# Optimization experiments

Measured on AMD Instinct MI355X. Metric: run time of the kernel, lower is better.

Reference implementation:

```python
import jax, jax.numpy as jnp
import numpy as np

LN_EPS = 1e-5
MASK_FILL = -1e9


def setup_inputs() -> dict:
    key = jax.random.key(0)
    ks = jax.random.split(key, 10)
    B, L, D, H, O, K = 128, 2048, 128, 256, 128, 64
    return {
        "sequence_emb": jax.random.normal(ks[0], (B, L, D), jnp.float32),
        "mask": jax.random.randint(ks[1], (B, L), 0, 2, jnp.int32),
        "target_emb": jax.random.normal(ks[2], (B, D), jnp.float32),
        "pos_table": jax.random.normal(ks[3], (10000, D), jnp.float32) * 0.02,
        "W_imp1": jax.random.normal(ks[4], (3 * D, H), jnp.float32) * (1.0 / np.sqrt(3 * D)),
        "b_imp1": jnp.zeros((H,), jnp.float32),
        "W_imp2": jax.random.normal(ks[5], (H, 1), jnp.float32) * (1.0 / np.sqrt(H)),
        "b_imp2": jnp.zeros((1,), jnp.float32),
        "W_enc1": jax.random.normal(ks[6], (2 * D, H), jnp.float32) * (1.0 / np.sqrt(2 * D)),
        "b_enc1": jnp.zeros((H,), jnp.float32),
        "W_enc2": jax.random.normal(ks[7], (H, O), jnp.float32) * (1.0 / np.sqrt(H)),
        "b_enc2": jnp.zeros((O,), jnp.float32),
        "ln_gamma": jnp.ones((O,), jnp.float32),
        "ln_beta": jnp.zeros((O,), jnp.float32),
        "top_k": K,
    }


def reference(sequence_emb, mask, target_emb, pos_table, W_imp1, b_imp1, W_imp2,
              b_imp2, W_enc1, b_enc1, W_enc2, b_enc2, ln_gamma, ln_beta, top_k):
    B, L, D = sequence_emb.shape
    # position embedding lookup (positions identical across batch -> keep (L,D) and broadcast)
    positions = jnp.minimum(jnp.arange(L), pos_table.shape[0] - 1)
    pos_emb = jnp.broadcast_to(pos_table[positions][None], (B, L, D))
    combined = jnp.concatenate([sequence_emb, pos_emb], axis=-1)          # (B,L,2D)
    tgt = jnp.broadcast_to(target_emb[:, None, :], (B, L, D))
    imp_in = jnp.concatenate([combined, tgt], axis=-1)                    # (B,L,3D)
    # importance MLP -> scalar score per event
    h = jax.nn.relu(imp_in @ W_imp1 + b_imp1)
    scores = (h @ W_imp2 + b_imp2)[..., 0]                                # (B,L)
    scores = jnp.where(mask == 0, MASK_FILL, scores)
    # masked top-k, then gather in chronological (sorted-index) order
    topk_values, topk_indices = jax.lax.top_k(scores, top_k)              # (B,K)
    idx_sorted = jnp.sort(topk_indices, axis=-1)
    sel = jnp.take_along_axis(combined, idx_sorted[..., None], axis=1)    # (B,K,2D)
    encoded = jax.nn.relu(sel @ W_enc1 + b_enc1) @ W_enc2 + b_enc2        # (B,K,O)
    # reorder scores to match sorted index order (torch: gather by argsort of indices)
    order = jnp.argsort(topk_indices, axis=-1)
    topk_scores = jnp.take_along_axis(topk_values, order, axis=-1)
    attn = jax.nn.softmax(topk_scores, axis=-1)                           # (B,K)
    pooled = jnp.einsum('bk,bkd->bd', attn, encoded)                      # (B,O)
    mu = jnp.mean(pooled, axis=-1, keepdims=True)
    var = jnp.var(pooled, axis=-1, keepdims=True)
    return (pooled - mu) * jax.lax.rsqrt(var + LN_EPS) * ln_gamma + ln_beta
```

## Files before the change

kernel.cpp:

```cpp
#include <hip/hip_runtime.h>
#include <hip/hip_bf16.h>

namespace {
constexpr int NB = 128;
constexpr int NL = 2048;
constexpr int ND = 128;
constexpr int NH = 256;
constexpr int NO = 128;
constexpr int NK = 64;
constexpr int MCAP = 192;
constexpr int HTHR = 96;
constexpr int BLOOP = 8;
constexpr float MASK_FILL_F = -1e9f;
constexpr float LN_EPS_F = 1e-5f;
}

typedef __attribute__((ext_vector_type(8))) short bf16x8;
typedef __attribute__((ext_vector_type(4))) float f32x4;

__device__ __forceinline__ unsigned short bf16rne(float x) {
  unsigned u = __float_as_uint(x);
  return (unsigned short)((u + 0x7FFFu + ((u >> 16) & 1u)) >> 16);
}

__global__ __launch_bounds__(256) void k_prep(
    const float* __restrict__ W1, const float* __restrict__ pos,
    const float* __restrict__ tgt, const float* __restrict__ b1,
    const float* __restrict__ We1, const float* __restrict__ We2,
    unsigned short* __restrict__ W1aT, float* __restrict__ P,
    float* __restrict__ T, unsigned short* __restrict__ We1T,
    unsigned short* __restrict__ We2T) {
  const int blk = blockIdx.x, t = threadIdx.x;
  if (blk < ND) {
    W1aT[(size_t)t * ND + blk] = bf16rne(W1[(size_t)blk * NH + t]);
    return;
  }
  if (blk >= ND + NL + NB) {
    const int b2 = blk - (ND + NL + NB);
    if (b2 < 256) {
      We1T[(size_t)t * 256 + b2] = bf16rne(We1[(size_t)b2 * NH + t]);
    } else {
      const int d = b2 - 256;
      if (t < NO) We2T[(size_t)t * 256 + d] = bf16rne(We2[(size_t)d * NO + t]);
    }
    return;
  }
  int r, w_off, add_bias;
  const float* src;
  float* out;
  if (blk < ND + NL) {
    r = blk - ND; src = pos; out = P; w_off = ND; add_bias = 1;
  } else {
    r = blk - (ND + NL); src = tgt; out = T; w_off = 2 * ND; add_bias = 0;
  }
  __shared__ float row[ND];
  if (t < ND) row[t] = src[(size_t)r * ND + t];
  __syncthreads();
  float acc = add_bias ? b1[t] : 0.0f;
#pragma unroll 8
  for (int d = 0; d < ND; ++d)
    acc = fmaf(row[d], W1[(size_t)(w_off + d) * NH + t], acc);
  out[(size_t)r * NH + t] = acc;
}

__global__ __launch_bounds__(512, 2) void k_scores_mfma(
    const float* __restrict__ seq, const int* __restrict__ mask,
    const unsigned short* __restrict__ W1aT, const float* __restrict__ w2,
    const float* __restrict__ b2, const float* __restrict__ b1,
    const float* __restrict__ T, float* __restrict__ scores) {
  const int l0 = blockIdx.x * 128;
  const int b0 = blockIdx.y * BLOOP;
  const int t = threadIdx.x;
  const int lane = t & 63;
  const int w = t >> 6;
  const int wh = w & 3;
  const int wl = w >> 2;
  const int lh = lane & 15;
  const int kq = lane >> 4;

  __shared__ unsigned short sSeq[2][128 * 128];
  __shared__ float sRed[4][128];

  bf16x8 a[4][4];
#pragma unroll
  for (int ks = 0; ks < 4; ++ks)
#pragma unroll
    for (int mt = 0; mt < 4; ++mt)
      a[ks][mt] = *(const bf16x8*)(
          W1aT + (size_t)(wh * 64 + mt * 16 + lh) * ND + ks * 32 + kq * 8);

  float4 wv[4], b1v[4];
#pragma unroll
  for (int mt = 0; mt < 4; ++mt) {
    wv[mt] = *(const float4*)(w2 + wh * 64 + mt * 16 + kq * 4);
    b1v[mt] = *(const float4*)(b1 + wh * 64 + mt * 16 + kq * 4);
  }
  const float b2v = b2[0];

  ushort4 pf[8];
  auto prefetch = [&](int bb) {
    const float4* g = (const float4*)(seq + ((size_t)bb * NL + l0) * ND);
#pragma unroll
    for (int i = 0; i < 8; ++i) {
      const float4 f = g[t + i * 512];
      pf[i].x = bf16rne(f.x); pf[i].y = bf16rne(f.y);
      pf[i].z = bf16rne(f.z); pf[i].w = bf16rne(f.w);
    }
  };
  auto commit = [&](unsigned short* dst) {
#pragma unroll
    for (int i = 0; i < 8; ++i) {
      const int v = t + i * 512;
      const int row = v >> 5;
      const int c8 = (v & 31) * 8;
      const int off = (row << 8) + (c8 ^ ((row & 15) << 4));
      *(ushort4*)((char*)dst + off) = pf[i];
    }
  };

  prefetch(b0);
  commit((unsigned short*)sSeq[0]);
  __syncthreads();

#pragma unroll 1
  for (int j = 0; j < BLOOP; ++j) {
    const int b = b0 + j;
    unsigned short* cSeq = (unsigned short*)sSeq[j & 1];
    unsigned short* nSeq = (unsigned short*)sSeq[(j & 1) ^ 1];

    if (j + 1 < BLOOP) prefetch(b + 1);

    float4 Tv[4];
#pragma unroll
    for (int mt = 0; mt < 4; ++mt)
      Tv[mt] = *(const float4*)(T + (size_t)b * NH + wh * 64 + mt * 16 + kq * 4);

    f32x4 acc[4][4];
#pragma unroll
    for (int mt = 0; mt < 4; ++mt)
#pragma unroll
      for (int nt = 0; nt < 4; ++nt) acc[mt][nt] = (f32x4){0.f, 0.f, 0.f, 0.f};

#pragma unroll
    for (int ks = 0; ks < 4; ++ks) {
      bf16x8 Bf[4];
#pragma unroll
      for (int nt = 0; nt < 4; ++nt) {
        const int row = wl * 64 + nt * 16 + lh;
        const int off = (row << 8) + (((ks << 6) + (kq << 4)) ^ ((row & 15) << 4));
        Bf[nt] = *(const bf16x8*)((const char*)cSeq + off);
      }
#pragma unroll
      for (int mt = 0; mt < 4; ++mt)
#pragma unroll
        for (int nt = 0; nt < 4; ++nt)
          acc[mt][nt] = __builtin_amdgcn_mfma_f32_16x16x32_bf16(
              a[ks][mt], Bf[nt], acc[mt][nt], 0, 0, 0);
    }
    __syncthreads();
    if (j + 1 < BLOOP) commit(nSeq);

    float p[4] = {0.f, 0.f, 0.f, 0.f};
#pragma unroll
    for (int mt = 0; mt < 4; ++mt) {
#pragma unroll
      for (int nt = 0; nt < 4; ++nt) {
        float z;
        z = acc[mt][nt][0] + Tv[mt].x + b1v[mt].x; p[nt] = fmaf(fmaxf(z, 0.f), wv[mt].x, p[nt]);
        z = acc[mt][nt][1] + Tv[mt].y + b1v[mt].y; p[nt] = fmaf(fmaxf(z, 0.f), wv[mt].y, p[nt]);
        z = acc[mt][nt][2] + Tv[mt].z + b1v[mt].z; p[nt] = fmaf(fmaxf(z, 0.f), wv[mt].z, p[nt]);
        z = acc[mt][nt][3] + Tv[mt].w + b1v[mt].w; p[nt] = fmaf(fmaxf(z, 0.f), wv[mt].w, p[nt]);
      }
    }
#pragma unroll
    for (int nt = 0; nt < 4; ++nt) {
      float v = p[nt];
      v += __shfl_xor(v, 16);
      v += __shfl_xor(v, 32);
      if (lane < 16) sRed[wh][wl * 64 + nt * 16 + lane] = v;
    }
    __syncthreads();
    if (t < 128) {
      const int l = l0 + t;
      float sc = sRed[0][t] + sRed[1][t] + sRed[2][t] + sRed[3][t] + b2v;
      if (mask[(size_t)b * NL + l] == 0) sc = MASK_FILL_F;
      scores[(size_t)b * NL + l] = sc;
    }
  }
}

__global__ __launch_bounds__(1024, 4) void k_select3(
    const float* __restrict__ scores, const float* __restrict__ seq,
    const int* __restrict__ mask, const float* __restrict__ W1,
    const float* __restrict__ w2, const float* __restrict__ b2,
    const float* __restrict__ P, const float* __restrict__ T,
    int* __restrict__ idx_sorted, float* __restrict__ attn) {
  const int b = blockIdx.x, t = threadIdx.x;
  __shared__ float s_stage[128 * ND];
  unsigned* hist = (unsigned*)s_stage;
  __shared__ unsigned chunk[256];
  __shared__ int sB;
  __shared__ unsigned sCntHi, sCntB, sN;
  __shared__ int s_cand[MCAP];
  __shared__ float s_cs[MCAP];
  __shared__ unsigned long long s_key[MCAP];
  __shared__ int sel_l[NK];
  __shared__ float sel_v[NK];
  __shared__ int srt_l[NK];
  __shared__ float srt_v[NK];

  for (int i = t; i < 4096; i += 1024) hist[i] = 0;
  if (t == 0) { sCntHi = 0; sCntB = 0; }
  __syncthreads();
  unsigned key2[2];
#pragma unroll
  for (int i = 0; i < 2; ++i) {
    unsigned u = __float_as_uint(scores[(size_t)b * NL + t + i * 1024]);
    u = (u & 0x80000000u) ? ~u : (u | 0x80000000u);
    key2[i] = u;
    atomicAdd(&hist[u >> 20], 1u);
  }
  __syncthreads();
  if (t < 256) {
    unsigned s = 0;
#pragma unroll 4
    for (int j = 0; j < 16; ++j) s += hist[t * 16 + j];
    chunk[t] = s;
  }
  __syncthreads();
  if (t == 0) {
    unsigned cum = 0;
    int c = 255;
    for (; c > 0; --c) {
      if (cum + chunk[c] >= (unsigned)HTHR) break;
      cum += chunk[c];
    }
    int bin = c * 16 + 15;
    for (; bin > c * 16; --bin) {
      if (cum + hist[bin] >= (unsigned)HTHR) break;
      cum += hist[bin];
    }
    sB = bin;
  }
  __syncthreads();
  const unsigned B = (unsigned)sB;
#pragma unroll
  for (int i = 0; i < 2; ++i) {
    if ((key2[i] >> 20) > B) {
      unsigned pos = atomicAdd(&sCntHi, 1u);
      s_cand[pos] = t + i * 1024;
    }
  }
  __syncthreads();
  const unsigned hi = sCntHi;
#pragma unroll
  for (int i = 0; i < 2; ++i) {
    if ((key2[i] >> 20) == B) {
      unsigned pos = atomicAdd(&sCntB, 1u);
      if (hi + pos < (unsigned)MCAP) s_cand[hi + pos] = t + i * 1024;
    }
  }
  __syncthreads();
  if (t == 0) {
    unsigned n = sCntHi + sCntB;
    sN = (n < (unsigned)MCAP) ? n : (unsigned)MCAP;
  }
  __syncthreads();
  const int n = (int)sN;

  const int hg = t & 63;
  const int rg = t >> 6;
  const float4* Wp = (const float4*)W1;
  const float4 wvq = ((const float4*)w2)[hg];
  const float4 Tvq = ((const float4*)(T + (size_t)b * NH))[hg];
  const float b2v = b2[0];
#pragma unroll 1
  for (int pass = 0; pass < 2; ++pass) {
    const int base = pass * 128;
    if (base >= n) break;
    __syncthreads();
#pragma unroll
    for (int i = 0; i < 4; ++i) {
      const int v = t + i * 1024;
      const int r = v >> 5, c = v & 31;
      const int slot = base + r;
      const int l = (slot < n) ? s_cand[slot] : 0;
      ((float4*)s_stage)[r * 32 + c] =
          ((const float4*)(seq + ((size_t)b * NL + l) * ND))[c];
    }
    __syncthreads();

    float acc[8][4];
#pragma unroll
    for (int r = 0; r < 8; ++r)
#pragma unroll
      for (int j = 0; j < 4; ++j) acc[r][j] = 0.0f;

    for (int d0 = 0; d0 < ND; d0 += 4) {
      float4 wq[4];
#pragma unroll
      for (int j = 0; j < 4; ++j) wq[j] = Wp[(size_t)(d0 + j) * (NH / 4) + hg];
#pragma unroll
      for (int r = 0; r < 8; ++r) {
        const float4 s = *(const float4*)&s_stage[(rg * 8 + r) * ND + d0];
        const float sv[4] = {s.x, s.y, s.z, s.w};
#pragma unroll
        for (int j = 0; j < 4; ++j) {
          acc[r][0] = fmaf(sv[j], wq[j].x, acc[r][0]);
          acc[r][1] = fmaf(sv[j], wq[j].y, acc[r][1]);
          acc[r][2] = fmaf(sv[j], wq[j].z, acc[r][2]);
          acc[r][3] = fmaf(sv[j], wq[j].w, acc[r][3]);
        }
      }
    }

#pragma unroll
    for (int r = 0; r < 8; ++r) {
      const int slot = base + rg * 8 + r;
      const int l = (slot < n) ? s_cand[slot] : 0;
      const float4 Pv = ((const float4*)(P + (size_t)l * NH))[hg];
      float z, p = 0.0f;
      z = acc[r][0] + Pv.x + Tvq.x; p = fmaf(fmaxf(z, 0.0f), wvq.x, p);
      z = acc[r][1] + Pv.y + Tvq.y; p = fmaf(fmaxf(z, 0.0f), wvq.y, p);
      z = acc[r][2] + Pv.z + Tvq.z; p = fmaf(fmaxf(z, 0.0f), wvq.z, p);
      z = acc[r][3] + Pv.w + Tvq.w; p = fmaf(fmaxf(z, 0.0f), wvq.w, p);
#pragma unroll
      for (int off = 32; off >= 1; off >>= 1) p += __shfl_xor(p, off);
      if (hg == 0 && slot < n) {
        float sc = p + b2v;
        if (mask[(size_t)b * NL + l] == 0) sc = MASK_FILL_F;
        s_cs[slot] = sc;
      }
    }
  }
  __syncthreads();

  for (int s = t; s < MCAP; s += 1024) {
    unsigned long long kk = 0ull;
    if (s < n) {
      unsigned u = __float_as_uint(s_cs[s]);
      u = (u & 0x80000000u) ? ~u : (u | 0x80000000u);
      const int l = s_cand[s];
      kk = ((unsigned long long)u << 11) | (unsigned long long)(NL - 1 - l);
    }
    s_key[s] = kk;
  }
  __syncthreads();
  for (int s = t; s < MCAP; s += 1024) {
    if (s < n) {
      const unsigned long long mk = s_key[s];
      int rank = 0;
      for (int j = 0; j < n; ++j) rank += (s_key[j] > mk) ? 1 : 0;
      if (rank < NK) {
        sel_l[rank] = (NL - 1) - (int)(mk & 0x7FFull);
        sel_v[rank] = s_cs[s];
      }
    }
  }
  __syncthreads();
  if (t < NK) {
    const int myl = sel_l[t];
    int pos = 0;
#pragma unroll 8
    for (int j = 0; j < NK; ++j) pos += (sel_l[j] < myl) ? 1 : 0;
    srt_l[pos] = myl;
    srt_v[pos] = sel_v[t];
  }
  __syncthreads();
  if (t < 64) {
    const float sc = srt_v[t];
    float m = sc;
#pragma unroll
    for (int off = 32; off >= 1; off >>= 1) m = fmaxf(m, __shfl_xor(m, off));
    const float e = expf(sc - m);
    float s = e;
#pragma unroll
    for (int off = 32; off >= 1; off >>= 1) s += __shfl_xor(s, off);
    attn[(size_t)b * NK + t] = e / s;
    idx_sorted[(size_t)b * NK + t] = srt_l[t];
  }
}

__global__ __launch_bounds__(512, 2) void k_encode(
    const float* __restrict__ seq, const float* __restrict__ pos,
    const int* __restrict__ idx_sorted, const float* __restrict__ attn_g,
    const unsigned short* __restrict__ We1T, const float* __restrict__ be1,
    const unsigned short* __restrict__ We2T, const float* __restrict__ be2,
    const float* __restrict__ gamma, const float* __restrict__ beta,
    float* __restrict__ out) {
  const int b = blockIdx.x, t = threadIdx.x;
  const int lane = t & 63, w = t >> 6;
  const int lh = lane & 15, kq = lane >> 4;
  __shared__ unsigned short s_in[64 * 256];
  __shared__ unsigned short s_h1[64 * 256];
  __shared__ float red[4][128];
  __shared__ float rr[4];
  __shared__ int s_idx[NK];
  __shared__ float s_at[NK];

  if (t < NK) {
    s_idx[t] = idx_sorted[(size_t)b * NK + t];
    s_at[t] = attn_g[(size_t)b * NK + t];
  }
  __syncthreads();

#pragma unroll
  for (int i = 0; i < 8; ++i) {
    const int v = t + i * 512;
    const int row = v >> 6;
    const int q = v & 63;
    const int idx = s_idx[row];
    float4 f;
    if (q < 32) f = ((const float4*)(seq + ((size_t)b * NL + idx) * ND))[q];
    else        f = ((const float4*)(pos + (size_t)idx * ND))[q - 32];
    ushort4 hv;
    hv.x = bf16rne(f.x); hv.y = bf16rne(f.y);
    hv.z = bf16rne(f.z); hv.w = bf16rne(f.w);
    const int off = (row << 9) + ((q * 8) ^ ((row & 15) << 4));
    *(ushort4*)((char*)s_in + off) = hv;
  }
  __syncthreads();

  {
    const int wh = w & 3, wn = w >> 2;
    f32x4 acc1[4][2];
#pragma unroll
    for (int mt = 0; mt < 4; ++mt)
#pragma unroll
      for (int nt = 0; nt < 2; ++nt) acc1[mt][nt] = (f32x4){0.f, 0.f, 0.f, 0.f};
#pragma unroll
    for (int ks = 0; ks < 8; ++ks) {
      bf16x8 Bf[2];
#pragma unroll
      for (int nt = 0; nt < 2; ++nt) {
        const int row = wn * 32 + nt * 16 + lh;
        const int off = (row << 9) + ((ks * 64 + kq * 16) ^ ((row & 15) << 4));
        Bf[nt] = *(const bf16x8*)((const char*)s_in + off);
      }
#pragma unroll
      for (int mt = 0; mt < 4; ++mt) {
        const bf16x8 Af = *(const bf16x8*)(
            We1T + (size_t)(wh * 64 + mt * 16 + lh) * 256 + ks * 32 + kq * 8);
#pragma unroll
        for (int nt = 0; nt < 2; ++nt)
          acc1[mt][nt] = __builtin_amdgcn_mfma_f32_16x16x32_bf16(
              Af, Bf[nt], acc1[mt][nt], 0, 0, 0);
      }
    }
#pragma unroll
    for (int mt = 0; mt < 4; ++mt) {
      const int h0 = wh * 64 + mt * 16 + kq * 4;
      const float4 bv = *(const float4*)(be1 + h0);
#pragma unroll
      for (int nt = 0; nt < 2; ++nt) {
        const int row = wn * 32 + nt * 16 + lh;
        const float z0 = fmaxf(acc1[mt][nt][0] + bv.x, 0.0f);
        const float z1 = fmaxf(acc1[mt][nt][1] + bv.y, 0.0f);
        const float z2 = fmaxf(acc1[mt][nt][2] + bv.z, 0.0f);
        const float z3 = fmaxf(acc1[mt][nt][3] + bv.w, 0.0f);
        const unsigned u0 = (unsigned)bf16rne(z0) | ((unsigned)bf16rne(z1) << 16);
        const unsigned u1 = (unsigned)bf16rne(z2) | ((unsigned)bf16rne(z3) << 16);
        const int off = (row << 9) + ((h0 * 2) ^ ((row & 15) << 4));
        *(unsigned*)((char*)s_h1 + off) = u0;
        *(unsigned*)((char*)s_h1 + off + 4) = u1;
      }
    }
  }
  __syncthreads();

  {
    const int wo = w & 1, wn4 = w >> 1;
    const int row = wn4 * 16 + lh;
    f32x4 acc2[4];
#pragma unroll
    for (int mt = 0; mt < 4; ++mt) acc2[mt] = (f32x4){0.f, 0.f, 0.f, 0.f};
#pragma unroll
    for (int ks = 0; ks < 8; ++ks) {
      const int off = (row << 9) + ((ks * 64 + kq * 16) ^ ((row & 15) << 4));
      const bf16x8 Bf = *(const bf16x8*)((const char*)s_h1 + off);
#pragma unroll
      for (int mt = 0; mt < 4; ++mt) {
        const bf16x8 Af = *(const bf16x8*)(
            We2T + (size_t)(wo * 64 + mt * 16 + lh) * 256 + ks * 32 + kq * 8);
        acc2[mt] = __builtin_amdgcn_mfma_f32_16x16x32_bf16(Af, Bf, acc2[mt], 0, 0, 0);
      }
    }
    const float at = s_at[row];
#pragma unroll
    for (int mt = 0; mt < 4; ++mt) {
#pragma unroll
      for (int j = 0; j < 4; ++j) {
        float v = acc2[mt][j] * at;
        v += __shfl_xor(v, 1);
        v += __shfl_xor(v, 2);
        v += __shfl_xor(v, 4);
        v += __shfl_xor(v, 8);
        if (lh == 0) red[wn4][wo * 64 + mt * 16 + kq * 4 + j] = v;
      }
    }
  }
  __syncthreads();

  float pooled = 0.0f;
  if (t < NO)
    pooled = red[0][t] + red[1][t] + red[2][t] + red[3][t] + be2[t];
  float s1 = (t < NO) ? pooled : 0.0f;
  float s2 = (t < NO) ? pooled * pooled : 0.0f;
#pragma unroll
  for (int off = 32; off >= 1; off >>= 1) {
    s1 += __shfl_xor(s1, off);
    s2 += __shfl_xor(s2, off);
  }
  if (t < NO && (t & 63) == 0) {
    rr[(t >> 6) * 2] = s1;
    rr[(t >> 6) * 2 + 1] = s2;
  }
  __syncthreads();
  if (t < NO) {
    const float S1 = rr[0] + rr[2];
    const float S2 = rr[1] + rr[3];
    const float mu = S1 / NO;
    const float var = S2 / NO - mu * mu;
    const float rs = rsqrtf(var + LN_EPS_F);
    out[(size_t)b * NO + t] = (pooled - mu) * rs * gamma[t] + beta[t];
  }
}

extern "C" void kernel_launch(void* const* d_in, const int* in_sizes, int n_in,
                              void* d_out, int out_size, void* d_ws, size_t ws_size,
                              hipStream_t stream) {
  (void)in_sizes; (void)n_in; (void)out_size; (void)ws_size;
  const float* seq = (const float*)d_in[0];
  const int* mask = (const int*)d_in[1];
  const float* tgt = (const float*)d_in[2];
  const float* pos = (const float*)d_in[3];
  const float* W1 = (const float*)d_in[4];
  const float* b1 = (const float*)d_in[5];
  const float* w2 = (const float*)d_in[6];
  const float* b2 = (const float*)d_in[7];
  const float* We1 = (const float*)d_in[8];
  const float* be1 = (const float*)d_in[9];
  const float* We2 = (const float*)d_in[10];
  const float* be2 = (const float*)d_in[11];
  const float* gam = (const float*)d_in[12];
  const float* bet = (const float*)d_in[13];
  float* out = (float*)d_out;

  float* P = (float*)d_ws;
  float* T = P + (size_t)NL * NH;
  float* scores = T + (size_t)NB * NH;
  float* attn = scores + (size_t)NB * NL;
  int* idxs = (int*)(attn + (size_t)NB * NK);
  unsigned short* w1aT = (unsigned short*)(idxs + (size_t)NB * NK);
  unsigned short* we1T = w1aT + (size_t)NH * ND;
  unsigned short* we2T = we1T + (size_t)256 * 256;

  k_prep<<<ND + NL + NB + 512, 256, 0, stream>>>(W1, pos, tgt, b1, We1, We2,
                                                 w1aT, P, T, we1T, we2T);
  k_scores_mfma<<<dim3(NL / 128, NB / BLOOP), 512, 0, stream>>>(
      seq, mask, w1aT, w2, b2, b1, T, scores);
  k_select3<<<NB, 1024, 0, stream>>>(scores, seq, mask, W1, w2, b2, P, T,
                                     idxs, attn);
  k_encode<<<NB, 512, 0, stream>>>(seq, pos, idxs, attn, we1T, be1, we2T, be2,
                                   gam, bet, out);
}
```

Measured before the change: 142.1 us.

## Fuse top-k selection and encoder into one tail kernel, skip masked scores

Merges the selection kernel and the encode kernel into a single 1024-thread kernel per batch row, so the sorted indices and attention weights stay in shared memory instead of going through global memory. A separate kernel launch is removed as well. The encoder GEMM is reworked for 16 waves, each handling one 16-row tile, and only 8 waves run the second GEMM. Masked positions are also left out of the histogram and candidate lists, which shrinks the candidate set. The risks are higher shared-memory use per block, which can lower occupancy, and different top-k behaviour when fewer than K unmasked entries exist.

```diff
diff --git a/kernel.cpp b/kernel.cpp
--- a/kernel.cpp
+++ b/kernel.cpp
@@ -189,13 +189,19 @@
   }
 }
 
-__global__ __launch_bounds__(1024, 4) void k_select3(
+__global__ __launch_bounds__(1024, 4) void k_tail(
     const float* __restrict__ scores, const float* __restrict__ seq,
     const int* __restrict__ mask, const float* __restrict__ W1,
     const float* __restrict__ w2, const float* __restrict__ b2,
     const float* __restrict__ P, const float* __restrict__ T,
-    int* __restrict__ idx_sorted, float* __restrict__ attn) {
+    const float* __restrict__ pos,
+    const unsigned short* __restrict__ We1T, const float* __restrict__ be1,
+    const unsigned short* __restrict__ We2T, const float* __restrict__ be2,
+    const float* __restrict__ gamma, const float* __restrict__ beta,
+    float* __restrict__ out) {
   const int b = blockIdx.x, t = threadIdx.x;
+  const int lane = t & 63, w = t >> 6;
+  const int lh = lane & 15, kq = lane >> 4;
   __shared__ float s_stage[128 * ND];
   unsigned* hist = (unsigned*)s_stage;
   __shared__ unsigned chunk[256];
@@ -208,7 +214,13 @@
   __shared__ float sel_v[NK];
   __shared__ int srt_l[NK];
   __shared__ float srt_v[NK];
-
+  __shared__ float s_at[NK];
+  __shared__ unsigned short s_in[64 * 256];
+  __shared__ unsigned short s_h1[64 * 256];
+  __shared__ float red[4][128];
+  __shared__ float rr[4];
+
+  const unsigned mkey = ~__float_as_uint(MASK_FILL_F);
   for (int i = t; i < 4096; i += 1024) hist[i] = 0;
   if (t == 0) { sCntHi = 0; sCntB = 0; }
   __syncthreads();
@@ -218,7 +230,7 @@
     unsigned u = __float_as_uint(scores[(size_t)b * NL + t + i * 1024]);
     u = (u & 0x80000000u) ? ~u : (u | 0x80000000u);
     key2[i] = u;
-    atomicAdd(&hist[u >> 20], 1u);
+    if (u != mkey) atomicAdd(&hist[u >> 20], 1u);
   }
   __syncthreads();
   if (t < 256) {
@@ -246,18 +258,18 @@
   const unsigned B = (unsigned)sB;
 #pragma unroll
   for (int i = 0; i < 2; ++i) {
-    if ((key2[i] >> 20) > B) {
-      unsigned pos = atomicAdd(&sCntHi, 1u);
-      s_cand[pos] = t + i * 1024;
+    if (key2[i] != mkey && (key2[i] >> 20) > B) {
+      unsigned pos_ = atomicAdd(&sCntHi, 1u);
+      s_cand[pos_] = t + i * 1024;
     }
   }
   __syncthreads();
   const unsigned hi = sCntHi;
 #pragma unroll
   for (int i = 0; i < 2; ++i) {
-    if ((key2[i] >> 20) == B) {
-      unsigned pos = atomicAdd(&sCntB, 1u);
-      if (hi + pos < (unsigned)MCAP) s_cand[hi + pos] = t + i * 1024;
+    if (key2[i] != mkey && (key2[i] >> 20) == B) {
+      unsigned pos_ = atomicAdd(&sCntB, 1u);
+      if (hi + pos_ < (unsigned)MCAP) s_cand[hi + pos_] = t + i * 1024;
     }
   }
   __syncthreads();
@@ -268,68 +280,70 @@
   __syncthreads();
   const int n = (int)sN;
 
-  const int hg = t & 63;
-  const int rg = t >> 6;
-  const float4* Wp = (const float4*)W1;
-  const float4 wvq = ((const float4*)w2)[hg];
-  const float4 Tvq = ((const float4*)(T + (size_t)b * NH))[hg];
-  const float b2v = b2[0];
+  {
+    const int hg = lane;
+    const int rg = w;
+    const float4* Wp = (const float4*)W1;
+    const float4 wvq = ((const float4*)w2)[hg];
+    const float4 Tvq = ((const float4*)(T + (size_t)b * NH))[hg];
+    const float b2v = b2[0];
 #pragma unroll 1
-  for (int pass = 0; pass < 2; ++pass) {
-    const int base = pass * 128;
-    if (base >= n) break;
-    __syncthreads();
-#pragma unroll
-    for (int i = 0; i < 4; ++i) {
-      const int v = t + i * 1024;
-      const int r = v >> 5, c = v & 31;
-      const int slot = base + r;
-      const int l = (slot < n) ? s_cand[slot] : 0;
-      ((float4*)s_stage)[r * 32 + c] =
-          ((const float4*)(seq + ((size_t)b * NL + l) * ND))[c];
-    }
-    __syncthreads();
-
-    float acc[8][4];
-#pragma unroll
-    for (int r = 0; r < 8; ++r)
-#pragma unroll
-      for (int j = 0; j < 4; ++j) acc[r][j] = 0.0f;
-
-    for (int d0 = 0; d0 < ND; d0 += 4) {
-      float4 wq[4];
-#pragma unroll
-      for (int j = 0; j < 4; ++j) wq[j] = Wp[(size_t)(d0 + j) * (NH / 4) + hg];
+    for (int pass = 0; pass < 2; ++pass) {
+      const int base = pass * 128;
+      if (base >= n) break;
+      __syncthreads();
+#pragma unroll
+      for (int i = 0; i < 4; ++i) {
+        const int v = t + i * 1024;
+        const int r = v >> 5, c = v & 31;
+        const int slot = base + r;
+        const int l = (slot < n) ? s_cand[slot] : 0;
+        ((float4*)s_stage)[r * 32 + c] =
+            ((const float4*)(seq + ((size_t)b * NL + l) * ND))[c];
+      }
+      __syncthreads();
+
+      float acc[8][4];
+#pragma unroll
+      for (int r = 0; r < 8; ++r)
+#pragma unroll
+        for (int j = 0; j < 4; ++j) acc[r][j] = 0.0f;
+
+      for (int d0 = 0; d0 < ND; d0 += 4) {
+        float4 wq[4];
+#pragma unroll
+        for (int j = 0; j < 4; ++j) wq[j] = Wp[(size_t)(d0 + j) * (NH / 4) + hg];
+#pragma unroll
+        for (int r = 0; r < 8; ++r) {
+          const float4 s = *(const float4*)&s_stage[(rg * 8 + r) * ND + d0];
+          const float sv[4] = {s.x, s.y, s.z, s.w};
+#pragma unroll
+          for (int j = 0; j < 4; ++j) {
+            acc[r][0] = fmaf(sv[j], wq[j].x, acc[r][0]);
+            acc[r][1] = fmaf(sv[j], wq[j].y, acc[r][1]);
+            acc[r][2] = fmaf(sv[j], wq[j].z, acc[r][2]);
+            acc[r][3] = fmaf(sv[j], wq[j].w, acc[r][3]);
+          }
+        }
+      }
+
 #pragma unroll
       for (int r = 0; r < 8; ++r) {
-        const float4 s = *(const float4*)&s_stage[(rg * 8 + r) * ND + d0];
-        const float sv[4] = {s.x, s.y, s.z, s.w};
-#pragma unroll
-        for (int j = 0; j < 4; ++j) {
-          acc[r][0] = fmaf(sv[j], wq[j].x, acc[r][0]);
-          acc[r][1] = fmaf(sv[j], wq[j].y, acc[r][1]);
-          acc[r][2] = fmaf(sv[j], wq[j].z, acc[r][2]);
-          acc[r][3] = fmaf(sv[j], wq[j].w, acc[r][3]);
+        const int slot = base + rg * 8 + r;
+        const int l = (slot < n) ? s_cand[slot] : 0;
+        const float4 Pv = ((const float4*)(P + (size_t)l * NH))[hg];
+        float z, p = 0.0f;
+        z = acc[r][0] + Pv.x + Tvq.x; p = fmaf(fmaxf(z, 0.0f), wvq.x, p);
+        z = acc[r][1] + Pv.y + Tvq.y; p = fmaf(fmaxf(z, 0.0f), wvq.y, p);
+        z = acc[r][2] + Pv.z + Tvq.z; p = fmaf(fmaxf(z, 0.0f), wvq.z, p);
+        z = acc[r][3] + Pv.w + Tvq.w; p = fmaf(fmaxf(z, 0.0f), wvq.w, p);
+#pragma unroll
+        for (int off = 32; off >= 1; off >>= 1) p += __shfl_xor(p, off);
+        if (hg == 0 && slot < n) {
+          float sc = p + b2v;
+          if (mask[(size_t)b * NL + l] == 0) sc = MASK_FILL_F;
+          s_cs[slot] = sc;
         }
-      }
-    }
-
-#pragma unroll
-    for (int r = 0; r < 8; ++r) {
-      const int slot = base + rg * 8 + r;
-      const int l = (slot < n) ? s_cand[slot] : 0;
-      const float4 Pv = ((const float4*)(P + (size_t)l * NH))[hg];
-      float z, p = 0.0f;
-      z = acc[r][0] + Pv.x + Tvq.x; p = fmaf(fmaxf(z, 0.0f), wvq.x, p);
-      z = acc[r][1] + Pv.y + Tvq.y; p = fmaf(fmaxf(z, 0.0f), wvq.y, p);
-      z = acc[r][2] + Pv.z + Tvq.z; p = fmaf(fmaxf(z, 0.0f), wvq.z, p);
-      z = acc[r][3] + Pv.w + Tvq.w; p = fmaf(fmaxf(z, 0.0f), wvq.w, p);
-#pragma unroll
-      for (int off = 32; off >= 1; off >>= 1) p += __shfl_xor(p, off);
-      if (hg == 0 && slot < n) {
-        float sc = p + b2v;
-        if (mask[(size_t)b * NL + l] == 0) sc = MASK_FILL_F;
-        s_cs[slot] = sc;
       }
     }
   }
@@ -360,11 +374,11 @@
   __syncthreads();
   if (t < NK) {
     const int myl = sel_l[t];
-    int pos = 0;
+    int pos_ = 0;
 #pragma unroll 8
-    for (int j = 0; j < NK; ++j) pos += (sel_l[j] < myl) ? 1 : 0;
-    srt_l[pos] = myl;
-    srt_v[pos] = sel_v[t];
+    for (int j = 0; j < NK; ++j) pos_ += (sel_l[j] < myl) ? 1 : 0;
+    srt_l[pos_] = myl;
+    srt_v[pos_] = sel_v[t];
   }
   __syncthreads();
   if (t < 64) {
@@ -376,40 +390,16 @@
     float s = e;
 #pragma unroll
     for (int off = 32; off >= 1; off >>= 1) s += __shfl_xor(s, off);
-    attn[(size_t)b * NK + t] = e / s;
-    idx_sorted[(size_t)b * NK + t] = srt_l[t];
-  }
-}
-
-__global__ __launch_bounds__(512, 2) void k_encode(
-    const float* __restrict__ seq, const float* __restrict__ pos,
-    const int* __restrict__ idx_sorted, const float* __restrict__ attn_g,
-    const unsigned short* __restrict__ We1T, const float* __restrict__ be1,
-    const unsigned short* __restrict__ We2T, const float* __restrict__ be2,
-    const float* __restrict__ gamma, const float* __restrict__ beta,
-    float* __restrict__ out) {
-  const int b = blockIdx.x, t = threadIdx.x;
-  const int lane = t & 63, w = t >> 6;
-  const int lh = lane & 15, kq = lane >> 4;
-  __shared__ unsigned short s_in[64 * 256];
-  __shared__ unsigned short s_h1[64 * 256];
-  __shared__ float red[4][128];
-  __shared__ float rr[4];
-  __shared__ int s_idx[NK];
-  __shared__ float s_at[NK];
-
-  if (t < NK) {
-    s_idx[t] = idx_sorted[(size_t)b * NK + t];
-    s_at[t] = attn_g[(size_t)b * NK + t];
-  }
-  __syncthreads();
-
-#pragma unroll
-  for (int i = 0; i < 8; ++i) {
-    const int v = t + i * 512;
+    s_at[t] = e / s;
+  }
+  __syncthreads();
+
+#pragma unroll
+  for (int i = 0; i < 4; ++i) {
+    const int v = t + i * 1024;
     const int row = v >> 6;
     const int q = v & 63;
-    const int idx = s_idx[row];
+    const int idx = srt_l[row];
     float4 f;
     if (q < 32) f = ((const float4*)(seq + ((size_t)b * NL + idx) * ND))[q];
     else        f = ((const float4*)(pos + (size_t)idx * ND))[q - 32];
@@ -423,52 +413,39 @@
 
   {
     const int wh = w & 3, wn = w >> 2;
-    f32x4 acc1[4][2];
-#pragma unroll
-    for (int mt = 0; mt < 4; ++mt)
-#pragma unroll
-      for (int nt = 0; nt < 2; ++nt) acc1[mt][nt] = (f32x4){0.f, 0.f, 0.f, 0.f};
+    const int row = wn * 16 + lh;
+    f32x4 acc1[4];
+#pragma unroll
+    for (int mt = 0; mt < 4; ++mt) acc1[mt] = (f32x4){0.f, 0.f, 0.f, 0.f};
 #pragma unroll
     for (int ks = 0; ks < 8; ++ks) {
-      bf16x8 Bf[2];
-#pragma unroll
-      for (int nt = 0; nt < 2; ++nt) {
-        const int row = wn * 32 + nt * 16 + lh;
-        const int off = (row << 9) + ((ks * 64 + kq * 16) ^ ((row & 15) << 4));
-        Bf[nt] = *(const bf16x8*)((const char*)s_in + off);
-      }
+      const int off = (row << 9) + ((ks * 64 + kq * 16) ^ ((row & 15) << 4));
+      const bf16x8 Bf = *(const bf16x8*)((const char*)s_in + off);
 #pragma unroll
       for (int mt = 0; mt < 4; ++mt) {
         const bf16x8 Af = *(const bf16x8*)(
             We1T + (size_t)(wh * 64 + mt * 16 + lh) * 256 + ks * 32 + kq * 8);
-#pragma unroll
-        for (int nt = 0; nt < 2; ++nt)
-          acc1[mt][nt] = __builtin_amdgcn_mfma_f32_16x16x32_bf16(
-              Af, Bf[nt], acc1[mt][nt], 0, 0, 0);
+        acc1[mt] = __builtin_amdgcn_mfma_f32_16x16x32_bf16(Af, Bf, acc1[mt], 0, 0, 0);
       }
     }
 #pragma unroll
     for (int mt = 0; mt < 4; ++mt) {
       const int h0 = wh * 64 + mt * 16 + kq * 4;
       const float4 bv = *(const float4*)(be1 + h0);
-#pragma unroll
-      for (int nt = 0; nt < 2; ++nt) {
-        const int row = wn * 32 + nt * 16 + lh;
-        const float z0 = fmaxf(acc1[mt][nt][0] + bv.x, 0.0f);
-        const float z1 = fmaxf(acc1[mt][nt][1] + bv.y, 0.0f);
-        const float z2 = fmaxf(acc1[mt][nt][2] + bv.z, 0.0f);
-        const float z3 = fmaxf(acc1[mt][nt][3] + bv.w, 0.0f);
-        const unsigned u0 = (unsigned)bf16rne(z0) | ((unsigned)bf16rne(z1) << 16);
-        const unsigned u1 = (unsigned)bf16rne(z2) | ((unsigned)bf16rne(z3) << 16);
-        const int off = (row << 9) + ((h0 * 2) ^ ((row & 15) << 4));
-        *(unsigned*)((char*)s_h1 + off) = u0;
-        *(unsigned*)((char*)s_h1 + off + 4) = u1;
-      }
-    }
-  }
-  __syncthreads();
-
-  {
+      const float z0 = fmaxf(acc1[mt][0] + bv.x, 0.0f);
+      const float z1 = fmaxf(acc1[mt][1] + bv.y, 0.0f);
+      const float z2 = fmaxf(acc1[mt][2] + bv.z, 0.0f);
+      const float z3 = fmaxf(acc1[mt][3] + bv.w, 0.0f);
+      const unsigned u0 = (unsigned)bf16rne(z0) | ((unsigned)bf16rne(z1) << 16);
+      const unsigned u1 = (unsigned)bf16rne(z2) | ((unsigned)bf16rne(z3) << 16);
+      const int off = (row << 9) + ((h0 * 2) ^ ((row & 15) << 4));
+      *(unsigned*)((char*)s_h1 + off) = u0;
+      *(unsigned*)((char*)s_h1 + off + 4) = u1;
+    }
+  }
+  __syncthreads();
+
+  if (w < 8) {
     const int wo = w & 1, wn4 = w >> 1;
     const int row = wn4 * 16 + lh;
     f32x4 acc2[4];
@@ -549,9 +526,7 @@
   float* P = (float*)d_ws;
   float* T = P + (size_t)NL * NH;
   float* scores = T + (size_t)NB * NH;
-  float* attn = scores + (size_t)NB * NL;
-  int* idxs = (int*)(attn + (size_t)NB * NK);
-  unsigned short* w1aT = (unsigned short*)(idxs + (size_t)NB * NK);
+  unsigned short* w1aT = (unsigned short*)(scores + (size_t)NB * NL);
   unsigned short* we1T = w1aT + (size_t)NH * ND;
   unsigned short* we2T = we1T + (size_t)256 * 256;
 
@@ -559,8 +534,6 @@
                                                  w1aT, P, T, we1T, we2T);
   k_scores_mfma<<<dim3(NL / 128, NB / BLOOP), 512, 0, stream>>>(
       seq, mask, w1aT, w2, b2, b1, T, scores);
-  k_select3<<<NB, 1024, 0, stream>>>(scores, seq, mask, W1, w2, b2, P, T,
-                                     idxs, attn);
-  k_encode<<<NB, 512, 0, stream>>>(seq, pos, idxs, attn, we1T, be1, we2T, be2,
-                                   gam, bet, out);
+  k_tail<<<NB, 1024, 0, stream>>>(scores, seq, mask, W1, w2, b2, P, T, pos,
+                                  we1T, be1, we2T, be2, gam, bet, out);
 }
```

Result: slower. 145.8 us (+2.6%).
